# Optimization experiments

Hardware: AMD Instinct MI355X
Metric: run time of the kernel (lower is better)

The kernel has to match this reference:

```python
import jax, jax.numpy as jnp
import numpy as np

NEG_INF = -1e20
SLOPE = 0.2  # LeakyReLU slope ('relu' init arg)
N_NODES, N_FEAT, N_HID, N_HEADS = 23, 1, 2, 2


def setup_inputs() -> dict:
    key = jax.random.key(0)
    ks = jax.random.split(key, 12)
    B = 16384
    node_attr_matrix = jax.random.normal(ks[0], (B, N_NODES, N_FEAT), dtype=jnp.float32)
    adjacency_matrix = jax.random.randint(ks[1], (B, N_NODES, N_NODES), 0, 2, dtype=jnp.int32)

    def xavier(k, shape, gain=1.414):
        fan_in, fan_out = shape[0], shape[1]
        lim = gain * np.sqrt(6.0 / (fan_in + fan_out))
        return jax.random.uniform(k, shape, jnp.float32, -lim, lim)

    return {
        "node_attr_matrix": node_attr_matrix,
        "adjacency_matrix": adjacency_matrix,
        "W0": xavier(ks[2], (N_FEAT, N_HID)),
        "a0": xavier(ks[3], (2 * N_HID, 1)),
        "W1": xavier(ks[4], (N_FEAT, N_HID)),
        "a1": xavier(ks[5], (2 * N_HID, 1)),
        "fc1_w": xavier(ks[6], (N_NODES * N_HID * N_HEADS, 128), gain=1.0),
        "fc1_b": jnp.zeros((128,), jnp.float32),
        "pre_w": xavier(ks[7], (128, 16), gain=1.0),
        "pre_b": jnp.zeros((16,), jnp.float32),
        "predict_w": xavier(ks[8], (16, 1), gain=1.0),
        "predict_b": jnp.zeros((1,), jnp.float32),
        "getvar_w": xavier(ks[9], (16, 1), gain=1.0),
        "getvar_b": jnp.zeros((1,), jnp.float32),
    }


def gat_layer(x, adj, W, a):
    # x: [B,N,Fin], adj: [B,N,N]
    h = jnp.matmul(x, W)  # [B,N,F]
    F_out = W.shape[1]
    # e[i,j] = leakyrelu(h_i . a[:F] + h_j . a[F:])  (avoids O(N^2*2F) concat)
    f1 = jnp.matmul(h, a[:F_out])            # [B,N,1]
    f2 = jnp.matmul(h, a[F_out:])            # [B,N,1]
    e = jax.nn.leaky_relu(f1 + jnp.swapaxes(f2, 1, 2), SLOPE)  # [B,N,N]
    e = jnp.where(adj > 0, e, NEG_INF)
    att = jax.nn.softmax(e, axis=1)          # NOTE: dim=1 as in the torch code
    h_prime = jnp.matmul(att, h)             # [B,N,F]
    return jax.nn.gelu(h_prime, approximate=False)  # concat=True branch


def reference(node_attr_matrix, adjacency_matrix, W0, a0, W1, a1,
              fc1_w, fc1_b, pre_w, pre_b, predict_w, predict_b,
              getvar_w, getvar_b):
    adj = adjacency_matrix.astype(jnp.float32)
    x = node_attr_matrix.astype(jnp.float32)[:, :N_NODES, :]
    # two attention heads, concatenated on feature dim
    x = jnp.concatenate([gat_layer(x, adj, W0, a0),
                         gat_layer(x, adj, W1, a1)], axis=2)  # [B,23,4]
    x = x.reshape(x.shape[0], -1)  # [B,92]
    xc = jax.nn.relu(x @ fc1_w + fc1_b)                 # fc1 (dropout off, eval)
    xp = jax.nn.gelu(xc @ pre_w + pre_b, approximate=False)  # pre
    y = jax.nn.relu(xp @ predict_w + predict_b)         # predict
    var = xp @ getvar_w + getvar_b                      # get_var
    return (y, var, xc)
```

## Files before the change

kernel.cpp:

```cpp
#include <hip/hip_runtime.h>
#include <hip/hip_bf16.h>

#define NN 23
#define BLK 256
#define SPB 8

__device__ __forceinline__ float lo2f(unsigned u) { return __uint_as_float(u << 16); }
__device__ __forceinline__ float hi2f(unsigned u) { return __uint_as_float(u & 0xFFFF0000u); }
__device__ __forceinline__ unsigned short f2b(float f) {
    union { __hip_bfloat16 h; unsigned short u; } c; c.h = __float2bfloat16(f); return c.u;
}
__device__ __forceinline__ float geluf(float v) {
    return 0.5f * v * (1.0f + erff(v * 0.70710678118654752f));
}

__global__ __launch_bounds__(BLK, 5) void gat_fused(
    const float* __restrict__ xattr, const int* __restrict__ adj,
    const float* __restrict__ W0,   const float* __restrict__ a0,
    const float* __restrict__ W1,   const float* __restrict__ a1,
    const float* __restrict__ fc1w, const float* __restrict__ fc1b,
    const float* __restrict__ prew, const float* __restrict__ preb,
    const float* __restrict__ predw, const float* __restrict__ predb,
    const float* __restrict__ varw,  const float* __restrict__ varb,
    float* __restrict__ outy, float* __restrict__ outv, float* __restrict__ outxc)
{
    __shared__ unsigned short s_w1[92 * 128];
    __shared__ unsigned s_pw[128 * 9];
    __shared__ float s_fc1b[128];
    __shared__ float s_aux[64];
    __shared__ float s_feat[SPB * 96];

    const int tid = threadIdx.x;

    for (int i = tid; i < (92 * 128) / 4; i += BLK) {
        float4 w = ((const float4*)fc1w)[i];
        unsigned lo = (unsigned)f2b(w.x) | ((unsigned)f2b(w.y) << 16);
        unsigned hi = (unsigned)f2b(w.z) | ((unsigned)f2b(w.w) << 16);
        *(uint2*)&s_w1[i * 4] = make_uint2(lo, hi);
    }
    for (int i = tid; i < 1024; i += BLK) {
        float2 w = ((const float2*)prew)[i];
        s_pw[(i >> 3) * 9 + (i & 7)] = (unsigned)f2b(w.x) | ((unsigned)f2b(w.y) << 16);
    }
    if (tid < 128) s_fc1b[tid] = fc1b[tid];
    if (tid < 16) {
        s_aux[12 + tid] = preb[tid];
        s_aux[28 + tid] = predw[tid];
        s_aux[44 + tid] = varw[tid];
    }
    if (tid == 0) {
        s_aux[0] = W0[0]; s_aux[1] = W0[1];
        s_aux[2] = a0[0]; s_aux[3] = a0[1]; s_aux[4] = a0[2]; s_aux[5] = a0[3];
        s_aux[6] = W1[0]; s_aux[7] = W1[1];
        s_aux[8] = a1[0]; s_aux[9] = a1[1]; s_aux[10] = a1[2]; s_aux[11] = a1[3];
        s_aux[60] = predb[0]; s_aux[61] = varb[0];
    }
    __syncthreads();

    const int slot = tid >> 5;
    const int l    = tid & 31;
    const int s    = blockIdx.x * SPB + slot;

    float xl = 0.0f;
    if (l < NN) xl = xattr[s * NN + l];
    float xv[NN];
    #pragma unroll
    for (int i = 0; i < NN; ++i) xv[i] = __shfl(xl, i, 32);

    unsigned cm = 0u;
    if (l < NN) {
        const int* ar = adj + (size_t)s * (NN * NN);
        #pragma unroll
        for (int i = 0; i < NN; ++i) cm |= (ar[i * NN + l] != 0) ? (1u << i) : 0u;
    }

    unsigned rm = 0u;
    #pragma unroll
    for (int i = 0; i < NN; ++i) {
        unsigned long long bal = __ballot((cm >> i) & 1u);
        unsigned half = (unsigned)(bal >> (tid & 32));
        rm = (l == i) ? half : rm;
    }
    unsigned em;
    {
        unsigned long long bal = __ballot(cm == 0u);
        em = ((unsigned)(bal >> (tid & 32))) & 0x7FFFFFu;
    }
    float sbase = 0.0f;
    #pragma unroll
    for (int j = 0; j < NN; ++j) sbase += ((em >> j) & 1u) ? xv[j] : 0.0f;
    sbase *= (1.0f / 23.0f);

    float fmine[4];
    #pragma unroll
    for (int h = 0; h < 2; ++h) {
        const float w0 = s_aux[h * 6 + 0], w1 = s_aux[h * 6 + 1];
        const float c1 = w0 * s_aux[h * 6 + 2] + w1 * s_aux[h * 6 + 3];
        const float c2 = w0 * s_aux[h * 6 + 4] + w1 * s_aux[h * 6 + 5];

        const float f2l = xl * c2;
        float dcol = 0.0f;
        #pragma unroll
        for (int i = 0; i < NN; ++i) {
            float e = fmaf(xv[i], c1, f2l);
            e = fmaxf(e, 0.2f * e);
            float t = ((cm >> i) & 1u) ? 1.0f : 0.0f;
            dcol = fmaf(__expf(e), t, dcol);
        }
        const float scl = (cm == 0u) ? 0.0f : __fdividef(xl, dcol);

        float sclv[NN];
        #pragma unroll
        for (int j = 0; j < NN; ++j) sclv[j] = __shfl(scl, j, 32);

        const float f1 = xl * c1;
        float sown = sbase;
        #pragma unroll
        for (int j = 0; j < NN; ++j) {
            float e = fmaf(xv[j], c2, f1);
            e = fmaxf(e, 0.2f * e);
            float t = ((rm >> j) & 1u) ? sclv[j] : 0.0f;
            sown = fmaf(__expf(e), t, sown);
        }

        fmine[h * 2 + 0] = geluf(w0 * sown);
        fmine[h * 2 + 1] = geluf(w1 * sown);
    }

    if (l < NN)
        *(float4*)&s_feat[slot * 96 + l * 4] = make_float4(fmine[0], fmine[1], fmine[2], fmine[3]);
    __syncthreads();

    const float* fL = &s_feat[slot * 96];
    const float4 b4 = *(const float4*)&s_fc1b[4 * l];
    float ac0 = b4.x, ac1 = b4.y, ac2 = b4.z, ac3 = b4.w;
    #pragma unroll
    for (int mq = 0; mq < 23; ++mq) {
        const float4 f4 = *(const float4*)&fL[mq * 4];
        #pragma unroll
        for (int u = 0; u < 4; ++u) {
            const float f = (u == 0) ? f4.x : (u == 1) ? f4.y : (u == 2) ? f4.z : f4.w;
            const uint2 wb = *(const uint2*)&s_w1[(mq * 4 + u) * 128 + 4 * l];
            ac0 = fmaf(f, lo2f(wb.x), ac0);
            ac1 = fmaf(f, hi2f(wb.x), ac1);
            ac2 = fmaf(f, lo2f(wb.y), ac2);
            ac3 = fmaf(f, hi2f(wb.y), ac3);
        }
    }
    const float r0 = fmaxf(ac0, 0.0f), r1 = fmaxf(ac1, 0.0f);
    const float r2 = fmaxf(ac2, 0.0f), r3 = fmaxf(ac3, 0.0f);
    *(float4*)&outxc[(size_t)s * 128 + 4 * l] = make_float4(r0, r1, r2, r3);

    float xp[16];
    #pragma unroll
    for (int t = 0; t < 16; ++t) xp[t] = 0.0f;
    #pragma unroll
    for (int c = 0; c < 4; ++c) {
        const float rr = (c == 0) ? r0 : (c == 1) ? r1 : (c == 2) ? r2 : r3;
        const unsigned* pw = &s_pw[(4 * l + c) * 9];
        #pragma unroll
        for (int u = 0; u < 8; ++u) {
            const unsigned w = pw[u];
            xp[2 * u + 0] = fmaf(rr, lo2f(w), xp[2 * u + 0]);
            xp[2 * u + 1] = fmaf(rr, hi2f(w), xp[2 * u + 1]);
        }
    }

    #pragma unroll
    for (int b = 3; b >= 0; --b) {
        const int m = 1 << b;
        #pragma unroll
        for (int k = 0; k < (1 << b); ++k) {
            float mine  = (l & m) ? xp[(1 << b) + k] : xp[k];
            float other = (l & m) ? xp[k] : xp[(1 << b) + k];
            xp[k] = mine + __shfl_xor(other, m, 32);
        }
    }
    xp[0] += __shfl_xor(xp[0], 16, 32);

    const int t2 = l & 15;
    const float g = geluf(xp[0] + s_aux[12 + t2]);
    float yp = g * s_aux[28 + t2];
    float vp = g * s_aux[44 + t2];
    #pragma unroll
    for (int m = 1; m < 16; m <<= 1) {
        yp += __shfl_xor(yp, m, 32);
        vp += __shfl_xor(vp, m, 32);
    }
    if (l == 0) {
        outy[s] = fmaxf(yp + s_aux[60], 0.0f);
        outv[s] = vp + s_aux[61];
    }
}

extern "C" void kernel_launch(void* const* d_in, const int* in_sizes, int n_in,
                              void* d_out, int out_size, void* d_ws, size_t ws_size,
                              hipStream_t stream) {
    const float* xattr = (const float*)d_in[0];
    const int*   adjp  = (const int*)d_in[1];

    const int B = in_sizes[0] / NN;
    float* o = (float*)d_out;
    float* outy  = o;
    float* outv  = o + B;
    float* outxc = o + 2 * (size_t)B;

    gat_fused<<<dim3(B / SPB), dim3(BLK), 0, stream>>>(
        xattr, adjp,
        (const float*)d_in[2], (const float*)d_in[3],
        (const float*)d_in[4], (const float*)d_in[5],
        (const float*)d_in[6], (const float*)d_in[7],
        (const float*)d_in[8], (const float*)d_in[9],
        (const float*)d_in[10], (const float*)d_in[11],
        (const float*)d_in[12], (const float*)d_in[13],
        outy, outv, outxc);
}
```

Baseline: 139.6 us.

## Use bf16 MFMA for fc1 and pre layers with 16 samples per block

Replaces the per-lane scalar FMA dot products for fc1 (92x128) and the pre layer (128x16) with 16x16x32 bf16 MFMA instructions. Weights are stored transposed and zero-padded in shared memory. Each block now handles 16 samples, with every 32-lane group running two attention rounds. The bf16 features and activations are staged in LDS for the second MFMA, which adds an extra barrier and loses some precision on the GAT outputs. Occupancy drops because of the larger LDS footprint and lower launch bounds, and the per-block weight conversion is amortized over more samples.

```diff
diff --git a/kernel.cpp b/kernel.cpp
--- a/kernel.cpp
+++ b/kernel.cpp
@@ -3,10 +3,13 @@
 
 #define NN 23
 #define BLK 256
-#define SPB 8
-
-__device__ __forceinline__ float lo2f(unsigned u) { return __uint_as_float(u << 16); }
-__device__ __forceinline__ float hi2f(unsigned u) { return __uint_as_float(u & 0xFFFF0000u); }
+#define SPB 16
+#define WST 104
+#define XST 136
+
+typedef __attribute__((ext_vector_type(8))) short bf16x8;
+typedef __attribute__((ext_vector_type(4))) float f32x4;
+
 __device__ __forceinline__ unsigned short f2b(float f) {
     union { __hip_bfloat16 h; unsigned short u; } c; c.h = __float2bfloat16(f); return c.u;
 }
@@ -14,7 +17,7 @@
     return 0.5f * v * (1.0f + erff(v * 0.70710678118654752f));
 }
 
-__global__ __launch_bounds__(BLK, 5) void gat_fused(
+__global__ __launch_bounds__(BLK, 4) void gat_fused(
     const float* __restrict__ xattr, const int* __restrict__ adj,
     const float* __restrict__ W0,   const float* __restrict__ a0,
     const float* __restrict__ W1,   const float* __restrict__ a1,
@@ -24,23 +27,30 @@
     const float* __restrict__ varw,  const float* __restrict__ varb,
     float* __restrict__ outy, float* __restrict__ outv, float* __restrict__ outxc)
 {
-    __shared__ unsigned short s_w1[92 * 128];
-    __shared__ unsigned s_pw[128 * 9];
+    __shared__ unsigned short s_w1t[128 * WST];
+    __shared__ unsigned short s_feat[SPB * WST];
+    __shared__ unsigned short s_xc[SPB * XST];
+    __shared__ unsigned short s_pwt[16 * XST];
     __shared__ float s_fc1b[128];
     __shared__ float s_aux[64];
-    __shared__ float s_feat[SPB * 96];
 
     const int tid = threadIdx.x;
 
-    for (int i = tid; i < (92 * 128) / 4; i += BLK) {
-        float4 w = ((const float4*)fc1w)[i];
-        unsigned lo = (unsigned)f2b(w.x) | ((unsigned)f2b(w.y) << 16);
-        unsigned hi = (unsigned)f2b(w.z) | ((unsigned)f2b(w.w) << 16);
-        *(uint2*)&s_w1[i * 4] = make_uint2(lo, hi);
-    }
-    for (int i = tid; i < 1024; i += BLK) {
-        float2 w = ((const float2*)prew)[i];
-        s_pw[(i >> 3) * 9 + (i & 7)] = (unsigned)f2b(w.x) | ((unsigned)f2b(w.y) << 16);
+    for (int i = tid; i < 92 * 128; i += BLK) {
+        const int m = i >> 7, n = i & 127;
+        s_w1t[n * WST + m] = f2b(fc1w[i]);
+    }
+    for (int i = tid; i < 256; i += BLK) {
+        const int n = i >> 1, u = i & 1;
+        *(unsigned*)&s_w1t[n * WST + 92 + 2 * u] = 0u;
+    }
+    if (tid < 32) {
+        const int r = tid >> 1, u = tid & 1;
+        *(unsigned*)&s_feat[r * WST + 92 + 2 * u] = 0u;
+    }
+    for (int i = tid; i < 2048; i += BLK) {
+        const int k = i >> 4, t = i & 15;
+        s_pwt[t * XST + k] = f2b(prew[i]);
     }
     if (tid < 128) s_fc1b[tid] = fc1b[tid];
     if (tid < 16) {
@@ -57,139 +67,153 @@
     }
     __syncthreads();
 
-    const int slot = tid >> 5;
-    const int l    = tid & 31;
-    const int s    = blockIdx.x * SPB + slot;
-
-    float xl = 0.0f;
-    if (l < NN) xl = xattr[s * NN + l];
-    float xv[NN];
-    #pragma unroll
-    for (int i = 0; i < NN; ++i) xv[i] = __shfl(xl, i, 32);
-
-    unsigned cm = 0u;
-    if (l < NN) {
-        const int* ar = adj + (size_t)s * (NN * NN);
-        #pragma unroll
-        for (int i = 0; i < NN; ++i) cm |= (ar[i * NN + l] != 0) ? (1u << i) : 0u;
-    }
-
-    unsigned rm = 0u;
-    #pragma unroll
-    for (int i = 0; i < NN; ++i) {
-        unsigned long long bal = __ballot((cm >> i) & 1u);
-        unsigned half = (unsigned)(bal >> (tid & 32));
-        rm = (l == i) ? half : rm;
-    }
-    unsigned em;
+    const int group = tid >> 5;
+    const int l     = tid & 31;
+
+    #pragma unroll 1
+    for (int rnd = 0; rnd < 2; ++rnd) {
+        const int sl = group * 2 + rnd;
+        const int s  = blockIdx.x * SPB + sl;
+
+        float xl = 0.0f;
+        if (l < NN) xl = xattr[s * NN + l];
+        float xv[NN];
+        #pragma unroll
+        for (int i = 0; i < NN; ++i) xv[i] = __shfl(xl, i, 32);
+
+        unsigned cm = 0u;
+        if (l < NN) {
+            const int* ar = adj + (size_t)s * (NN * NN);
+            #pragma unroll
+            for (int i = 0; i < NN; ++i) cm |= (ar[i * NN + l] != 0) ? (1u << i) : 0u;
+        }
+        unsigned rm = 0u;
+        #pragma unroll
+        for (int i = 0; i < NN; ++i) {
+            unsigned long long bal = __ballot((cm >> i) & 1u);
+            unsigned half = (unsigned)(bal >> (tid & 32));
+            rm = (l == i) ? half : rm;
+        }
+        unsigned em;
+        {
+            unsigned long long bal = __ballot(cm == 0u);
+            em = ((unsigned)(bal >> (tid & 32))) & 0x7FFFFFu;
+        }
+        float sbase = 0.0f;
+        #pragma unroll
+        for (int j = 0; j < NN; ++j) sbase += ((em >> j) & 1u) ? xv[j] : 0.0f;
+        sbase *= (1.0f / 23.0f);
+
+        float fmine[4];
+        #pragma unroll
+        for (int h = 0; h < 2; ++h) {
+            const float w0 = s_aux[h * 6 + 0], w1 = s_aux[h * 6 + 1];
+            const float c1 = w0 * s_aux[h * 6 + 2] + w1 * s_aux[h * 6 + 3];
+            const float c2 = w0 * s_aux[h * 6 + 4] + w1 * s_aux[h * 6 + 5];
+
+            const float f2l = xl * c2;
+            float dcol = 0.0f;
+            #pragma unroll
+            for (int i = 0; i < NN; ++i) {
+                float e = fmaf(xv[i], c1, f2l);
+                e = fmaxf(e, 0.2f * e);
+                float t = ((cm >> i) & 1u) ? 1.0f : 0.0f;
+                dcol = fmaf(__expf(e), t, dcol);
+            }
+            const float scl = (cm == 0u) ? 0.0f : __fdividef(xl, dcol);
+
+            float sclv[NN];
+            #pragma unroll
+            for (int j = 0; j < NN; ++j) sclv[j] = __shfl(scl, j, 32);
+
+            const float f1 = xl * c1;
+            float sown = sbase;
+            #pragma unroll
+            for (int j = 0; j < NN; ++j) {
+                float e = fmaf(xv[j], c2, f1);
+                e = fmaxf(e, 0.2f * e);
+                float t = ((rm >> j) & 1u) ? sclv[j] : 0.0f;
+                sown = fmaf(__expf(e), t, sown);
+            }
+            fmine[h * 2 + 0] = geluf(w0 * sown);
+            fmine[h * 2 + 1] = geluf(w1 * sown);
+        }
+
+        if (l < NN) {
+            unsigned lo = (unsigned)f2b(fmine[0]) | ((unsigned)f2b(fmine[1]) << 16);
+            unsigned hi = (unsigned)f2b(fmine[2]) | ((unsigned)f2b(fmine[3]) << 16);
+            *(uint2*)&s_feat[sl * WST + 4 * l] = make_uint2(lo, hi);
+        }
+    }
+    __syncthreads();
+
     {
-        unsigned long long bal = __ballot(cm == 0u);
-        em = ((unsigned)(bal >> (tid & 32))) & 0x7FFFFFu;
-    }
-    float sbase = 0.0f;
-    #pragma unroll
-    for (int j = 0; j < NN; ++j) sbase += ((em >> j) & 1u) ? xv[j] : 0.0f;
-    sbase *= (1.0f / 23.0f);
-
-    float fmine[4];
-    #pragma unroll
-    for (int h = 0; h < 2; ++h) {
-        const float w0 = s_aux[h * 6 + 0], w1 = s_aux[h * 6 + 1];
-        const float c1 = w0 * s_aux[h * 6 + 2] + w1 * s_aux[h * 6 + 3];
-        const float c2 = w0 * s_aux[h * 6 + 4] + w1 * s_aux[h * 6 + 5];
-
-        const float f2l = xl * c2;
-        float dcol = 0.0f;
-        #pragma unroll
-        for (int i = 0; i < NN; ++i) {
-            float e = fmaf(xv[i], c1, f2l);
-            e = fmaxf(e, 0.2f * e);
-            float t = ((cm >> i) & 1u) ? 1.0f : 0.0f;
-            dcol = fmaf(__expf(e), t, dcol);
-        }
-        const float scl = (cm == 0u) ? 0.0f : __fdividef(xl, dcol);
-
-        float sclv[NN];
-        #pragma unroll
-        for (int j = 0; j < NN; ++j) sclv[j] = __shfl(scl, j, 32);
-
-        const float f1 = xl * c1;
-        float sown = sbase;
-        #pragma unroll
-        for (int j = 0; j < NN; ++j) {
-            float e = fmaf(xv[j], c2, f1);
-            e = fmaxf(e, 0.2f * e);
-            float t = ((rm >> j) & 1u) ? sclv[j] : 0.0f;
-            sown = fmaf(__expf(e), t, sown);
-        }
-
-        fmine[h * 2 + 0] = geluf(w0 * sown);
-        fmine[h * 2 + 1] = geluf(w1 * sown);
-    }
-
-    if (l < NN)
-        *(float4*)&s_feat[slot * 96 + l * 4] = make_float4(fmine[0], fmine[1], fmine[2], fmine[3]);
+        const int wave = tid >> 6;
+        const int lane = tid & 63;
+        const int q    = lane >> 4;
+        const int c16  = lane & 15;
+
+        f32x4 acc0 = {0.f, 0.f, 0.f, 0.f};
+        f32x4 acc1 = {0.f, 0.f, 0.f, 0.f};
+        const int n0 = 32 * wave + c16;
+        const int n1 = n0 + 16;
+        #pragma unroll
+        for (int t = 0; t < 3; ++t) {
+            const bf16x8 a  = *(const bf16x8*)&s_feat[c16 * WST + 32 * t + 8 * q];
+            const bf16x8 b0 = *(const bf16x8*)&s_w1t[n0 * WST + 32 * t + 8 * q];
+            const bf16x8 b1 = *(const bf16x8*)&s_w1t[n1 * WST + 32 * t + 8 * q];
+            acc0 = __builtin_amdgcn_mfma_f32_16x16x32_bf16(a, b0, acc0, 0, 0, 0);
+            acc1 = __builtin_amdgcn_mfma_f32_16x16x32_bf16(a, b1, acc1, 0, 0, 0);
+        }
+        const float bia0 = s_fc1b[n0], bia1 = s_fc1b[n1];
+        const size_t gbase = (size_t)blockIdx.x * SPB * 128;
+        #pragma unroll
+        for (int r = 0; r < 4; ++r) {
+            const int srow = 4 * q + r;
+            const float v0 = fmaxf(acc0[r] + bia0, 0.0f);
+            const float v1 = fmaxf(acc1[r] + bia1, 0.0f);
+            outxc[gbase + (size_t)srow * 128 + n0] = v0;
+            outxc[gbase + (size_t)srow * 128 + n1] = v1;
+            s_xc[srow * XST + n0] = f2b(v0);
+            s_xc[srow * XST + n1] = f2b(v1);
+        }
+    }
     __syncthreads();
 
-    const float* fL = &s_feat[slot * 96];
-    const float4 b4 = *(const float4*)&s_fc1b[4 * l];
-    float ac0 = b4.x, ac1 = b4.y, ac2 = b4.z, ac3 = b4.w;
-    #pragma unroll
-    for (int mq = 0; mq < 23; ++mq) {
-        const float4 f4 = *(const float4*)&fL[mq * 4];
-        #pragma unroll
-        for (int u = 0; u < 4; ++u) {
-            const float f = (u == 0) ? f4.x : (u == 1) ? f4.y : (u == 2) ? f4.z : f4.w;
-            const uint2 wb = *(const uint2*)&s_w1[(mq * 4 + u) * 128 + 4 * l];
-            ac0 = fmaf(f, lo2f(wb.x), ac0);
-            ac1 = fmaf(f, hi2f(wb.x), ac1);
-            ac2 = fmaf(f, lo2f(wb.y), ac2);
-            ac3 = fmaf(f, hi2f(wb.y), ac3);
-        }
-    }
-    const float r0 = fmaxf(ac0, 0.0f), r1 = fmaxf(ac1, 0.0f);
-    const float r2 = fmaxf(ac2, 0.0f), r3 = fmaxf(ac3, 0.0f);
-    *(float4*)&outxc[(size_t)s * 128 + 4 * l] = make_float4(r0, r1, r2, r3);
-
-    float xp[16];
-    #pragma unroll
-    for (int t = 0; t < 16; ++t) xp[t] = 0.0f;
-    #pragma unroll
-    for (int c = 0; c < 4; ++c) {
-        const float rr = (c == 0) ? r0 : (c == 1) ? r1 : (c == 2) ? r2 : r3;
-        const unsigned* pw = &s_pw[(4 * l + c) * 9];
-        #pragma unroll
-        for (int u = 0; u < 8; ++u) {
-            const unsigned w = pw[u];
-            xp[2 * u + 0] = fmaf(rr, lo2f(w), xp[2 * u + 0]);
-            xp[2 * u + 1] = fmaf(rr, hi2f(w), xp[2 * u + 1]);
-        }
-    }
-
-    #pragma unroll
-    for (int b = 3; b >= 0; --b) {
-        const int m = 1 << b;
-        #pragma unroll
-        for (int k = 0; k < (1 << b); ++k) {
-            float mine  = (l & m) ? xp[(1 << b) + k] : xp[k];
-            float other = (l & m) ? xp[k] : xp[(1 << b) + k];
-            xp[k] = mine + __shfl_xor(other, m, 32);
-        }
-    }
-    xp[0] += __shfl_xor(xp[0], 16, 32);
-
-    const int t2 = l & 15;
-    const float g = geluf(xp[0] + s_aux[12 + t2]);
-    float yp = g * s_aux[28 + t2];
-    float vp = g * s_aux[44 + t2];
-    #pragma unroll
-    for (int m = 1; m < 16; m <<= 1) {
-        yp += __shfl_xor(yp, m, 32);
-        vp += __shfl_xor(vp, m, 32);
-    }
-    if (l == 0) {
-        outy[s] = fmaxf(yp + s_aux[60], 0.0f);
-        outv[s] = vp + s_aux[61];
+    if (tid < 64) {
+        const int q   = tid >> 4;
+        const int c16 = tid & 15;
+        f32x4 acc = {0.f, 0.f, 0.f, 0.f};
+        #pragma unroll
+        for (int t = 0; t < 4; ++t) {
+            const bf16x8 a = *(const bf16x8*)&s_xc[c16 * XST + 32 * t + 8 * q];
+            const bf16x8 b = *(const bf16x8*)&s_pwt[c16 * XST + 32 * t + 8 * q];
+            acc = __builtin_amdgcn_mfma_f32_16x16x32_bf16(a, b, acc, 0, 0, 0);
+        }
+        const float pb = s_aux[12 + c16], pw = s_aux[28 + c16], vw = s_aux[44 + c16];
+        float yp[4], vp[4];
+        #pragma unroll
+        for (int r = 0; r < 4; ++r) {
+            const float g = geluf(acc[r] + pb);
+            yp[r] = g * pw;
+            vp[r] = g * vw;
+        }
+        #pragma unroll
+        for (int m = 1; m < 16; m <<= 1) {
+            #pragma unroll
+            for (int r = 0; r < 4; ++r) {
+                yp[r] += __shfl_xor(yp[r], m, 64);
+                vp[r] += __shfl_xor(vp[r], m, 64);
+            }
+        }
+        if (c16 == 0) {
+            const int sb = blockIdx.x * SPB + 4 * q;
+            #pragma unroll
+            for (int r = 0; r < 4; ++r) {
+                outy[sb + r] = fmaxf(yp[r] + s_aux[60], 0.0f);
+                outv[sb + r] = vp[r] + s_aux[61];
+            }
+        }
     }
 }
 
```

Result: faster. 119.8 us (-14.2%).
